# Kernel optimization log

Measured on AMD Instinct MI355X. Metric: run time of the kernel, lower is better.

The kernel has to match this reference:

```python
import jax, jax.numpy as jnp
import numpy as np

B, S, D, H = 2, 2048, 1024, 16
HEAD_DIM = D // H
THETA = 10000.0


def setup_inputs() -> dict:
    key = jax.random.key(0)
    kx, kq, kk, kv, ko = jax.random.split(key, 5)
    w_scale = jnp.float32(D ** -0.5)  # keep logits O(1)
    return {
        "x": jax.random.normal(kx, (B, S, D), dtype=jnp.float32),
        "WQ": jax.random.normal(kq, (D, D), dtype=jnp.float32) * w_scale,
        "WK": jax.random.normal(kk, (D, D), dtype=jnp.float32) * w_scale,
        "WV": jax.random.normal(kv, (D, D), dtype=jnp.float32) * w_scale,
        "WO": jax.random.normal(ko, (D, D), dtype=jnp.float32) * w_scale,
        "token_positions": jnp.arange(S, dtype=jnp.int32),
    }


def _rope(x, pos, theta):
    # x: [B, H, S, dh]; pos: [S]. Interleaved (even, odd) pair rotation.
    dh = x.shape[-1]
    inv_freq = theta ** (-jnp.arange(0, dh, 2, dtype=jnp.float32) / dh)  # [dh/2]
    ang = pos.astype(jnp.float32)[:, None] * inv_freq                    # [S, dh/2]
    cos, sin = jnp.cos(ang), jnp.sin(ang)
    x1, x2 = x[..., 0::2], x[..., 1::2]
    r1 = x1 * cos - x2 * sin
    r2 = x1 * sin + x2 * cos
    return jnp.stack([r1, r2], axis=-1).reshape(x.shape)


def reference(x, WQ, WK, WV, WO, token_positions):
    Bs, Ss, Dm = x.shape
    dh = Dm // H
    # QKV projections (Linear with no bias, y = x @ W.T), split heads -> [B,H,S,dh]
    q = (x @ WQ.T).reshape(Bs, Ss, H, dh).transpose(0, 2, 1, 3)
    k = (x @ WK.T).reshape(Bs, Ss, H, dh).transpose(0, 2, 1, 3)
    v = (x @ WV.T).reshape(Bs, Ss, H, dh).transpose(0, 2, 1, 3)
    q = _rope(q, token_positions, THETA)
    k = _rope(k, token_positions, THETA)
    scores = jnp.einsum("bhqd,bhkd->bhqk", q, k) * jnp.float32(dh ** -0.5)
    causal = jnp.tril(jnp.ones((Ss, Ss), dtype=bool))
    scores = jnp.where(causal, scores, jnp.finfo(scores.dtype).min)
    attn = jax.nn.softmax(scores, axis=-1)
    out = jnp.einsum("bhqk,bhkd->bhqd", attn, v)
    out = out.transpose(0, 2, 1, 3).reshape(Bs, Ss, Dm)
    return out @ WO.T
```

## Files before the change

kernel.cpp:

```cpp
#include <hip/hip_runtime.h>
#include <hip/hip_bf16.h>


#define S_LEN 2048
#define NEG_SENT -30000.0f

typedef __attribute__((ext_vector_type(8))) short short8;
typedef __attribute__((ext_vector_type(4))) float f32x4;
typedef unsigned int u32;
typedef unsigned short u16;

static __device__ __forceinline__ float bf2f(u16 u) {
  union { u32 i; float f; } v; v.i = ((u32)u) << 16; return v.f;
}
static __device__ __forceinline__ u16 f2bf(float f) {
  union { float f; u32 i; } v; v.f = f;
  u32 u = v.i;
  u32 r = (u + 0x7fffu + ((u >> 16) & 1u)) >> 16;
  return (u16)r;
}
static __device__ __forceinline__ u32 cvtpk(float a, float b) {
  u32 r;
  asm("v_cvt_pk_bf16_f32 %0, %1, %2" : "=v"(r) : "v"(a), "v"(b));
  return r;
}

static __device__ __forceinline__ void glds16(const void* g, void* l) {
  __builtin_amdgcn_global_load_lds((const __attribute__((address_space(1))) u32*)g,
                                   (__attribute__((address_space(3))) u32*)l, 16, 0, 0);
}

__global__ void convert_kernel(const float* __restrict__ x, const float* __restrict__ wq,
                               const float* __restrict__ wk, const float* __restrict__ wv,
                               const float* __restrict__ wo, const int* __restrict__ pos,
                               u16* __restrict__ xb, u16* __restrict__ wb,
                               float2* __restrict__ tab) {
  const int stride = gridDim.x * blockDim.x;
  for (int i = blockIdx.x * blockDim.x + threadIdx.x; i < 2162688; i += stride) {
    if (i >= 2097152) {
      int e = i - 2097152;
      int s = e >> 5, ip = e & 31;
      float p = (float)pos[s];
      float ang = p * __builtin_exp2f((float)ip * -0.41524101186f);
      float sn, cs;
      sincosf(ang, &sn, &cs);
      tab[e] = make_float2(cs, sn);
      continue;
    }
    const float* src; u16* dst; int off;
    if (i < 1048576) { src = x; dst = xb; off = i; }
    else {
      int j = i - 1048576;
      int widx = j >> 18;
      off = j & 262143;
      src = (widx == 0) ? wq : (widx == 1) ? wk : (widx == 2) ? wv : wo;
      dst = wb + (size_t)widx * 1048576;
    }
    float4 v = ((const float4*)src)[off];
    ushort4 o;
    o.x = f2bf(v.x); o.y = f2bf(v.y); o.z = f2bf(v.z); o.w = f2bf(v.w);
    ((ushort4*)dst)[off] = o;
  }
}

template <int OUTMODE>
__global__ __launch_bounds__(256, 2) void gemm_bt(const u16* __restrict__ A,
                                                  const u16* __restrict__ B,
                                                  u16* __restrict__ o0, u16* __restrict__ o1,
                                                  u16* __restrict__ o2, float* __restrict__ oF,
                                                  const float2* __restrict__ tab, int K) {
  __shared__ __align__(16) u16 AsBs[2 * 128 * 64];
  u16* const As = AsBs;
  u16* const Bs = AsBs + 128 * 64;
  const int tid = threadIdx.x, w = tid >> 6, l = tid & 63, l15 = l & 15, l4 = l >> 4;
  const int wr = w >> 1, wc = w & 1;
  const int lid = blockIdx.y * gridDim.x + blockIdx.x;
  const int xcd = lid & 7;
  const int jj2 = lid >> 3;
  const int mrows = gridDim.y >> 3;
  const int m0 = (xcd * mrows + jj2 / gridDim.x) << 7;
  const int n0 = (jj2 % gridDim.x) << 7;
  const int r = tid >> 3;
  const int swcol = ((tid & 7) << 4) ^ ((r & 7) << 4);
  const char* Ag = (const char*)A + (((size_t)(m0 + r) * K) << 1) + swcol;
  const char* Bg = (const char*)B + (((size_t)(n0 + r) * K) << 1) + swcol;
  char* AsW = (char*)As + (w << 10);
  char* BsW = (char*)Bs + (w << 10);
  const size_t rowskip = ((size_t)32 * K) << 1;
  f32x4 acc[4][4] = {};
  for (int k0 = 0; k0 < K; k0 += 64) {
    __syncthreads();
    const size_t kb = (size_t)k0 << 1;
#pragma unroll
    for (int i = 0; i < 4; i++) {
      glds16(Ag + kb + (size_t)i * rowskip, AsW + i * 4096);
      glds16(Bg + kb + (size_t)i * rowskip, BsW + i * 4096);
    }
    __syncthreads();
#pragma unroll
    for (int kk = 0; kk < 2; kk++) {
      short8 a[4], b[4];
#pragma unroll
      for (int m = 0; m < 4; m++) {
        int row = (wr << 6) + (m << 4) + l15;
        a[m] = *(const short8*)((const char*)As + row * 128 +
                                (((kk << 6) + (l4 << 4)) ^ ((row & 7) << 4)));
      }
#pragma unroll
      for (int n = 0; n < 4; n++) {
        int row = (wc << 6) + (n << 4) + l15;
        b[n] = *(const short8*)((const char*)Bs + row * 128 +
                                (((kk << 6) + (l4 << 4)) ^ ((row & 7) << 4)));
      }
#pragma unroll
      for (int m = 0; m < 4; m++)
#pragma unroll
        for (int n = 0; n < 4; n++)
          acc[m][n] = __builtin_amdgcn_mfma_f32_16x16x32_bf16(a[m], b[n], acc[m][n], 0, 0, 0);
    }
  }
  if (OUTMODE == 0 && n0 >= 2048) {
    __syncthreads();
    u16* T = AsBs;
#pragma unroll
    for (int m = 0; m < 4; m++)
#pragma unroll
      for (int n = 0; n < 4; n++) {
        int ct = (wc << 6) + (n << 4) + l15;
#pragma unroll
        for (int j = 0; j < 4; j++) {
          int rt = (wr << 6) + (m << 4) + (l4 << 2) + j;
          T[rt * 128 + (ct ^ (((rt >> 6) & 1) << 1))] = f2bf(acc[m][n][j]);
        }
      }
    __syncthreads();
    const int d = tid >> 1, sh = tid & 1;
    const int dr = d ^ (sh << 1);
    const int bb = m0 >> 11;
    const int colv = (n0 & 1023) + d;
    const int row = (((bb << 4) | (colv >> 6)) << 6) | (colv & 63);
    u16* dst = o2 + ((size_t)row << 11) + (m0 & (S_LEN - 1)) + (sh << 6);
#pragma unroll
    for (int k8 = 0; k8 < 8; k8++) {
      u16 tmp[8];
#pragma unroll
      for (int e = 0; e < 8; e++) tmp[e] = T[((sh << 6) + (k8 << 3) + e) * 128 + dr];
      *(uint4*)(dst + (k8 << 3)) = *(const uint4*)tmp;
    }
    return;
  }
#pragma unroll
  for (int m = 0; m < 4; m++) {
    int grow_b = m0 + (wr << 6) + (m << 4) + (l4 << 2);
#pragma unroll
    for (int n = 0; n < 4; n++) {
      int gcol = n0 + (wc << 6) + (n << 4) + l15;
      if (OUTMODE == 1) {
#pragma unroll
        for (int j = 0; j < 4; j++)
          oF[((size_t)(grow_b + j) << 10) + gcol] = acc[m][n][j];
      } else {
        const float qscale = (gcol < 1024) ? 0.125f * 1.44269504089f : 1.f;
        u16* base = (gcol < 1024) ? o0 : o1;
        const int col = gcol & 1023;
        const int d = col & 63;
        const float sgn = (d & 1) ? 1.f : -1.f;
        const int ip = d >> 1;
#pragma unroll
        for (int j = 0; j < 4; j++) {
          int grow = grow_b + j;
          float v = acc[m][n][j] * qscale;
          float pv = __shfl_xor(v, 1, 64);
          float2 cssn = tab[((grow & (S_LEN - 1)) << 5) + ip];
          base[((size_t)grow << 10) + col] = f2bf(v * cssn.x + pv * cssn.y * sgn);
        }
      }
    }
  }
}

__global__ __launch_bounds__(768, 3) void attn_kernel(const u16* __restrict__ Q,
                                                      const u16* __restrict__ K,
                                                      const u16* __restrict__ Vt,
                                                      u16* __restrict__ O) {
  extern __shared__ __align__(16) char smem[];
  const int tid = threadIdx.x, w = tid >> 6, l = tid & 63, l15 = l & 15, g = l >> 4;
  const int grp = tid >> 8, w4 = (tid >> 6) & 3;
  const int i = blockIdx.x;
  const int xcd = i & 7, slot = i >> 3;
  const int bh = ((slot >> 3) << 3) | xcd;
  const int p = slot & 7;
  const int b = bh >> 4, h = bh & 15;
  const int swz = (l15 & 7) << 4;

  const int gt = tid & 255;
  const int r = gt >> 3;
  const int swc = ((gt & 7) << 4) ^ ((r & 7) << 4);
  const char* Kg = (const char*)K + ((size_t)(b * S_LEN + r) << 11) + (h << 7) + swc;
  const char* Vg = (const char*)Vt + ((size_t)((bh << 6) + r) << 12) + swc;
  char* const KsG = smem + grp * 32768;
  char* const VsG = smem + grp * 32768 + 16384;
  char* const Pw = smem + 98304 + (w << 11);
  float* const oMrg1 = (float*)smem;
  float* const oMrg2 = (float*)(smem + 32768);
  float* const lMrg = (float*)(smem + 122880);

#define STAGE(T, BSEL)                                              \
  do {                                                              \
    char* kd = KsG + ((BSEL) << 13) + (w4 << 10);                   \
    char* vd = VsG + ((BSEL) << 13) + (w4 << 10);                   \
    const char* ks = Kg + ((size_t)(T) << 17);                      \
    const char* vs = Vg + ((T) << 7);                               \
    glds16(ks, kd);                                                 \
    glds16(ks + (32 << 11), kd + 4096);                             \
    glds16(vs, vd);                                                 \
    glds16(vs + ((size_t)32 << 12), vd + 4096);                     \
  } while (0)

  auto run_qt = [&](int qt) {
    const int q0 = qt << 7;
    const int nt = (qt + 1) << 1;
    const int nr = (nt + 2) / 3;

    short8 aQ[2][2];
    {
      const int qrow0 = q0 + (w4 << 5) + l15;
      const u16* qp = Q + (((size_t)(b * S_LEN + qrow0)) << 10) + (h << 6) + (g << 3);
      aQ[0][0] = *(const short8*)qp;
      aQ[0][1] = *(const short8*)(qp + 32);
      aQ[1][0] = *(const short8*)(qp + (16 << 10));
      aQ[1][1] = *(const short8*)(qp + (16 << 10) + 32);
    }
    f32x4 o[2][4] = {};
    float l_r[2] = {0.f, 0.f};

    auto subtile = [&](int t, const char* Kbuf, const char* Vbuf, bool domask) {
      f32x4 s[2][4] = {};
#pragma unroll
      for (int kk = 0; kk < 2; ++kk) {
        short8 aK[4];
#pragma unroll
        for (int n = 0; n < 4; ++n) {
          int row = (n << 4) + l15;
          aK[n] = *(const short8*)(Kbuf + row * 128 + (((kk << 6) + (g << 4)) ^ swz));
        }
        __builtin_amdgcn_s_setprio(1);
#pragma unroll
        for (int n = 0; n < 4; ++n) {
          s[0][n] = __builtin_amdgcn_mfma_f32_16x16x32_bf16(aK[n], aQ[0][kk], s[0][n], 0, 0, 0);
          s[1][n] = __builtin_amdgcn_mfma_f32_16x16x32_bf16(aK[n], aQ[1][kk], s[1][n], 0, 0, 0);
        }
        __builtin_amdgcn_s_setprio(0);
      }
      if (domask) {
#pragma unroll
        for (int qs = 0; qs < 2; ++qs) {
          int qg = q0 + (w4 << 5) + (qs << 4) + l15;
#pragma unroll
          for (int n = 0; n < 4; ++n)
#pragma unroll
            for (int jj = 0; jj < 4; ++jj) {
              int key = (t << 6) + (n << 4) + (g << 2) + jj;
              if (key > qg) s[qs][n][jj] = NEG_SENT;
            }
        }
      }
      short8 aP[2][2];
#pragma unroll
      for (int qs = 0; qs < 2; ++qs) {
        float rs = 0.f;
        u32 pk[8];
#pragma unroll
        for (int n = 0; n < 4; ++n) {
          float p0 = __builtin_exp2f(s[qs][n][0]);
          float p1 = __builtin_exp2f(s[qs][n][1]);
          float p2 = __builtin_exp2f(s[qs][n][2]);
          float p3 = __builtin_exp2f(s[qs][n][3]);
          rs += (p0 + p1) + (p2 + p3);
          pk[2 * n] = cvtpk(p0, p1);
          pk[2 * n + 1] = cvtpk(p2, p3);
        }
        l_r[qs] += rs;
        char* pr = Pw + l15 * 128;
#pragma unroll
        for (int n = 0; n < 4; ++n) {
          uint2 pv;
          pv.x = pk[2 * n];
          pv.y = pk[2 * n + 1];
          *(uint2*)(pr + (((n << 5) + (g << 3)) ^ swz)) = pv;
        }
#pragma unroll
        for (int kk = 0; kk < 2; ++kk)
          aP[qs][kk] = *(const short8*)(pr + (((kk << 6) + (g << 4)) ^ swz));
      }
#pragma unroll
      for (int kk = 0; kk < 2; ++kk) {
        int co = (kk << 6) + (g << 4);
        __builtin_amdgcn_s_setprio(1);
#pragma unroll
        for (int nd = 0; nd < 4; ++nd) {
          int row = (nd << 4) + l15;
          short8 bV = *(const short8*)(Vbuf + row * 128 + (co ^ swz));
          o[0][nd] = __builtin_amdgcn_mfma_f32_16x16x32_bf16(aP[0][kk], bV, o[0][nd], 0, 0, 0);
          o[1][nd] = __builtin_amdgcn_mfma_f32_16x16x32_bf16(aP[1][kk], bV, o[1][nd], 0, 0, 0);
        }
        __builtin_amdgcn_s_setprio(0);
      }
    };

    if (grp < nt) STAGE(grp, 0);
    __syncthreads();

    for (int rr = 0; rr < nr; ++rr) {
      const int bsel = rr & 1;
      const int t = 3 * rr + grp;
      if (t + 3 < nt) STAGE(t + 3, bsel ^ 1);
      if (t < nt) {
        subtile(t, KsG + (bsel << 13), VsG + (bsel << 13), t >= nt - 2);
      }
      __syncthreads();
    }

    if (grp >= 1) {
      float* ob = ((grp == 1) ? oMrg1 : oMrg2) + (w4 << 11);
#pragma unroll
      for (int qs = 0; qs < 2; ++qs)
#pragma unroll
        for (int nd = 0; nd < 4; ++nd)
          *(f32x4*)(ob + (((qs << 2) | nd) << 8) + (l << 2)) = o[qs][nd];
      float* lb = lMrg + ((grp - 1) << 9) + (w4 << 7);
      lb[l] = l_r[0];
      lb[64 + l] = l_r[1];
    }
    __syncthreads();
    if (grp == 0) {
      float* ob1 = oMrg1 + (w4 << 11);
      float* ob2 = oMrg2 + (w4 << 11);
      float* lb1 = lMrg + (w4 << 7);
      float* lb2 = lMrg + 512 + (w4 << 7);
#pragma unroll
      for (int qs = 0; qs < 2; ++qs) {
        float lsum = l_r[qs] + lb1[(qs << 6) + l] + lb2[(qs << 6) + l];
        lsum += __shfl_xor(lsum, 16);
        lsum += __shfl_xor(lsum, 32);
        float linv = 1.f / lsum;
        f32x4 oB1[4], oB2[4];
#pragma unroll
        for (int nd = 0; nd < 4; ++nd) {
          oB1[nd] = *(const f32x4*)(ob1 + (((qs << 2) | nd) << 8) + (l << 2));
          oB2[nd] = *(const f32x4*)(ob2 + (((qs << 2) | nd) << 8) + (l << 2));
        }
#pragma unroll
        for (int jj = 0; jj < 4; ++jj) {
          float lo = __shfl(linv, (g << 2) + jj, 16);
          int qg = q0 + (w4 << 5) + (qs << 4) + (g << 2) + jj;
          u16* orow = O + (((size_t)(b * S_LEN + qg)) << 10) + (h << 6) + l15;
#pragma unroll
          for (int nd = 0; nd < 4; ++nd)
            orow[nd << 4] = f2bf((o[qs][nd][jj] + oB1[nd][jj] + oB2[nd][jj]) * lo);
        }
      }
    }
    __syncthreads();
  };

  run_qt(p);
  run_qt(15 - p);
#undef STAGE
}

extern "C" void kernel_launch(void* const* d_in, const int* in_sizes, int n_in,
                              void* d_out, int out_size, void* d_ws, size_t ws_size,
                              hipStream_t stream) {
  (void)in_sizes; (void)n_in; (void)out_size; (void)ws_size;
  const float* x = (const float*)d_in[0];
  const float* wq = (const float*)d_in[1];
  const float* wk = (const float*)d_in[2];
  const float* wv = (const float*)d_in[3];
  const float* wo = (const float*)d_in[4];
  const int* pos = (const int*)d_in[5];
  char* ws = (char*)d_ws;
  u16* xb = (u16*)ws;
  u16* wb = (u16*)(ws + ((size_t)8 << 20));
  u16* Qb = (u16*)(ws + ((size_t)16 << 20));
  u16* Kb = (u16*)(ws + ((size_t)24 << 20));
  u16* Vtg = (u16*)(ws + ((size_t)32 << 20));
  u16* Ab = (u16*)(ws + ((size_t)40 << 20));
  float* out = (float*)d_out;
  float2* tab = (float2*)d_out;

  convert_kernel<<<2112, 256, 0, stream>>>(x, wq, wk, wv, wo, pos, xb, wb, tab);
  dim3 g1(24, 32);
  gemm_bt<0><<<g1, 256, 0, stream>>>(xb, wb, Qb, Kb, Vtg, nullptr, tab, 1024);
  attn_kernel<<<256, 768, 126976, stream>>>(Qb, Kb, Vtg, Ab);
  dim3 g3(8, 32);
  gemm_bt<1><<<g3, 256, 0, stream>>>(Ab, wb + (size_t)3 * 1048576, nullptr, nullptr, nullptr,
                                     out, nullptr, 1024);
}
```

Measured before the change: 102.2 us.

## Load K and V fragments directly from global memory instead of LDS staging

```diff
diff --git a/kernel.cpp b/kernel.cpp
--- a/kernel.cpp
+++ b/kernel.cpp
@@ -193,29 +193,13 @@
   const int b = bh >> 4, h = bh & 15;
   const int swz = (l15 & 7) << 4;
 
-  const int gt = tid & 255;
-  const int r = gt >> 3;
-  const int swc = ((gt & 7) << 4) ^ ((r & 7) << 4);
-  const char* Kg = (const char*)K + ((size_t)(b * S_LEN + r) << 11) + (h << 7) + swc;
-  const char* Vg = (const char*)Vt + ((size_t)((bh << 6) + r) << 12) + swc;
-  char* const KsG = smem + grp * 32768;
-  char* const VsG = smem + grp * 32768 + 16384;
-  char* const Pw = smem + 98304 + (w << 11);
-  float* const oMrg1 = (float*)smem;
-  float* const oMrg2 = (float*)(smem + 32768);
-  float* const lMrg = (float*)(smem + 122880);
-
-#define STAGE(T, BSEL)                                              \
-  do {                                                              \
-    char* kd = KsG + ((BSEL) << 13) + (w4 << 10);                   \
-    char* vd = VsG + ((BSEL) << 13) + (w4 << 10);                   \
-    const char* ks = Kg + ((size_t)(T) << 17);                      \
-    const char* vs = Vg + ((T) << 7);                               \
-    glds16(ks, kd);                                                 \
-    glds16(ks + (32 << 11), kd + 4096);                             \
-    glds16(vs, vd);                                                 \
-    glds16(vs + ((size_t)32 << 12), vd + 4096);                     \
-  } while (0)
+  char* const Pw = smem + (w << 11);
+  float* const oMrg1 = (float*)(smem + 24576);
+  float* const oMrg2 = (float*)(smem + 57344);
+  float* const lMrg = (float*)(smem + 90112);
+
+  const u16* const Kbase = K + (((size_t)(b * S_LEN + l15)) << 10) + (h << 6) + (g << 3);
+  const u16* const Vbase = Vt + (((size_t)((bh << 6) + l15)) << 11) + (g << 3);
 
   auto run_qt = [&](int qt) {
     const int q0 = qt << 7;
@@ -234,16 +218,16 @@
     f32x4 o[2][4] = {};
     float l_r[2] = {0.f, 0.f};
 
-    auto subtile = [&](int t, const char* Kbuf, const char* Vbuf, bool domask) {
+    auto subtile = [&](int t, bool domask) {
+      const u16* Kt_ = Kbase + ((size_t)t << 16);
+      const u16* Vt_ = Vbase + (t << 6);
       f32x4 s[2][4] = {};
 #pragma unroll
       for (int kk = 0; kk < 2; ++kk) {
         short8 aK[4];
 #pragma unroll
-        for (int n = 0; n < 4; ++n) {
-          int row = (n << 4) + l15;
-          aK[n] = *(const short8*)(Kbuf + row * 128 + (((kk << 6) + (g << 4)) ^ swz));
-        }
+        for (int n = 0; n < 4; ++n)
+          aK[n] = *(const short8*)(Kt_ + (n << 14) + (kk << 5));
         __builtin_amdgcn_s_setprio(1);
 #pragma unroll
         for (int n = 0; n < 4; ++n) {
@@ -295,12 +279,10 @@
       }
 #pragma unroll
       for (int kk = 0; kk < 2; ++kk) {
-        int co = (kk << 6) + (g << 4);
         __builtin_amdgcn_s_setprio(1);
 #pragma unroll
         for (int nd = 0; nd < 4; ++nd) {
-          int row = (nd << 4) + l15;
-          short8 bV = *(const short8*)(Vbuf + row * 128 + (co ^ swz));
+          short8 bV = *(const short8*)(Vt_ + ((size_t)nd << 15) + (kk << 5));
           o[0][nd] = __builtin_amdgcn_mfma_f32_16x16x32_bf16(aP[0][kk], bV, o[0][nd], 0, 0, 0);
           o[1][nd] = __builtin_amdgcn_mfma_f32_16x16x32_bf16(aP[1][kk], bV, o[1][nd], 0, 0, 0);
         }
@@ -308,19 +290,12 @@
       }
     };
 
-    if (grp < nt) STAGE(grp, 0);
-    __syncthreads();
-
     for (int rr = 0; rr < nr; ++rr) {
-      const int bsel = rr & 1;
       const int t = 3 * rr + grp;
-      if (t + 3 < nt) STAGE(t + 3, bsel ^ 1);
-      if (t < nt) {
-        subtile(t, KsG + (bsel << 13), VsG + (bsel << 13), t >= nt - 2);
-      }
-      __syncthreads();
-    }
-
+      if (t < nt) subtile(t, t >= nt - 2);
+    }
+
+    __syncthreads();
     if (grp >= 1) {
       float* ob = ((grp == 1) ? oMrg1 : oMrg2) + (w4 << 11);
 #pragma unroll
@@ -366,7 +341,6 @@
 
   run_qt(p);
   run_qt(15 - p);
-#undef STAGE
 }
 
 extern "C" void kernel_launch(void* const* d_in, const int* in_sizes, int n_in,
@@ -392,7 +366,7 @@
   convert_kernel<<<2112, 256, 0, stream>>>(x, wq, wk, wv, wo, pos, xb, wb, tab);
   dim3 g1(24, 32);
   gemm_bt<0><<<g1, 256, 0, stream>>>(xb, wb, Qb, Kb, Vtg, nullptr, tab, 1024);
-  attn_kernel<<<256, 768, 126976, stream>>>(Qb, Kb, Vtg, Ab);
+  attn_kernel<<<256, 768, 94208, stream>>>(Qb, Kb, Vtg, Ab);
   dim3 g3(8, 32);
   gemm_bt<1><<<g3, 256, 0, stream>>>(Ab, wb + (size_t)3 * 1048576, nullptr, nullptr, nullptr,
                                      out, nullptr, 1024);
```

Result: slower. 132.8 us (+30.0%).
